# Kernel optimization log

Measured on AMD Instinct MI355X. Metric: run time of the kernel, lower is better.

The kernel has to match this reference:

```python
import jax, jax.numpy as jnp
import numpy as np

N = 64          # SSM state size
L = 8192        # l_max / sequence length
BATCH = 2048


def setup_inputs() -> dict:
    key = jax.random.key(0)
    k1, k2, k3, k4, k5 = jax.random.split(key, 5)
    u = jax.random.normal(k1, (BATCH, L), dtype=jnp.float32)
    # lecun_normal: std = 1/sqrt(fan_in), fan_in = dim -2
    A = jax.random.normal(k2, (N, N), dtype=jnp.float32) / np.sqrt(N)
    B = jax.random.normal(k3, (N, 1), dtype=jnp.float32) / np.sqrt(N)
    C = jax.random.normal(k4, (1, N), dtype=jnp.float32)  # fan_in = 1
    D = jnp.ones((1,), dtype=jnp.float32)
    # log_step_initializer: log-uniform over [1e-3, 1e-1]
    lo, hi = np.log(0.001), np.log(0.1)
    log_step = (jax.random.uniform(k5, (1,)) * (hi - lo) + lo).astype(jnp.float32)
    return {"u": u, "A": A, "B": B, "C": C, "D": D, "log_step": log_step}


def _ssm_forward(u, A, B, C, D, log_step):
    n_state = A.shape[0]
    seq_len = u.shape[-1]
    step = jnp.exp(log_step)  # (1,)
    # Bilinear discretization: Ab = (I - s/2 A)^-1 (I + s/2 A); Bb = s (I - s/2 A)^-1 B
    I = jnp.eye(n_state, dtype=A.dtype)
    half = (step / 2.0) * A
    BL = jnp.linalg.inv(I - half)
    Ab = BL @ (I + half)            # (N, N)
    Bb = (step * BL) @ B            # (N, 1)
    # K_conv: K[l] = C @ Ab^l @ Bb, computed with a scan (x_{l+1} = Ab x_l)
    def kstep(x, _):
        y = (C @ x)[0]              # scalar
        return Ab @ x, y
    _, K = jax.lax.scan(kstep, Bb[:, 0], None, length=seq_len)  # (L,)
    # Causal convolution via FFT with zero padding to 2L (matches jnp.pad + rfft)
    nfft = 2 * seq_len
    ud = jnp.fft.rfft(u, n=nfft, axis=-1)    # (BATCH, L+1) complex
    Kd = jnp.fft.rfft(K, n=nfft)             # (L+1,) complex, shared over batch
    y = jnp.fft.irfft(ud * Kd, n=nfft, axis=-1)[..., :seq_len]
    return y + D * u


def reference(u, A, B, C, D, log_step):
    return _ssm_forward(u, A, B, C, D, log_step)
```

## Files before the change

kernel.cpp:

```cpp
#include <hip/hip_runtime.h>
#include <math.h>

#define LSEQ   8192
#define CHUNK  64
#define NCHUNK 128
#define NBATCH 2048
#define NGRP   16
#define GLEN   8

#define WS_E   0
#define WS_SG  (NBATCH * NGRP * 64)
#define T0     (NBATCH * NCHUNK * 64)
#define WS_WH  (T0 + 8256)
#define WS_WL  (T0 + 12352)
#define WS_PH  (T0 + 16448)
#define WS_PL  (T0 + 18496)
#define WS_A1H (T0 + 20544)
#define WS_A1L (T0 + 22592)
#define WS_PGH (T0 + 24640)
#define WS_PGL (T0 + 26688)

typedef short bf16x8 __attribute__((ext_vector_type(8)));
typedef float f32x4  __attribute__((ext_vector_type(4)));
typedef unsigned short u16;

__device__ __forceinline__ u16 bf16rne(float x) {
  unsigned b = __builtin_bit_cast(unsigned, x);
  return (u16)((b + 0x7fffu + ((b >> 16) & 1u)) >> 16);
}
__device__ __forceinline__ float bf2f(u16 h) {
  return __builtin_bit_cast(float, ((unsigned)h) << 16);
}
__device__ __forceinline__ void split2(float x, u16& h, u16& l) {
  h = bf16rne(x);
  l = bf16rne(x - bf2f(h));
}
__device__ __forceinline__ void split3(float x, u16& h, u16& m, u16& l) {
  h = bf16rne(x);
  float r = x - bf2f(h);
  m = bf16rne(r);
  r -= bf2f(m);
  l = bf16rne(r);
}

__device__ __forceinline__ int sinv(int c) {
  return (c & 0x23) | ((c & 4) << 2) | ((c & 0x18) >> 1);
}

__device__ __forceinline__ int swz(int r, int c) {
  return r * 64 + (c ^ ((r & 7) << 3));
}
__device__ __forceinline__ float tri_get(const u16* p, int r, int c) {
  const int e = swz(r, c);
  return bf2f(p[e]) + bf2f(p[4096 + e]) + bf2f(p[8192 + e]);
}

__device__ __forceinline__ void mfma_tile3(
    const u16* __restrict__ A3, const u16* __restrict__ B3, u16* __restrict__ D3,
    int mt, int nt, int aShift,
    const u16* add1, const u16* add2, int addI, int rLo, int rHi) {
  const int lane = threadIdx.x & 63;
  const int n = lane & 15, q = lane >> 4;
  int ar = mt * 16 + n - aShift;
  ar = ar < 0 ? 0 : (ar > 63 ? 63 : ar);
  const int bc = nt * 16 + n;
  bf16x8 ah[2], am[2], al[2], bh[2], bm[2], bl[2];
#pragma unroll
  for (int ks = 0; ks < 2; ++ks) {
    const int ao = swz(ar, ks * 32 + q * 8);
    const int bo = swz(bc, ks * 32 + q * 8);
    ah[ks] = *(const bf16x8*)(A3 + ao);
    am[ks] = *(const bf16x8*)(A3 + 4096 + ao);
    al[ks] = *(const bf16x8*)(A3 + 8192 + ao);
    bh[ks] = *(const bf16x8*)(B3 + bo);
    bm[ks] = *(const bf16x8*)(B3 + 4096 + bo);
    bl[ks] = *(const bf16x8*)(B3 + 8192 + bo);
  }
  f32x4 acc = {0.f, 0.f, 0.f, 0.f};
#define MF(a, b) acc = __builtin_amdgcn_mfma_f32_16x16x32_bf16(a, b, acc, 0, 0, 0)
  MF(ah[0], bh[0]); MF(ah[1], bh[1]);
  MF(ah[0], bm[0]); MF(ah[1], bm[1]);
  MF(am[0], bh[0]); MF(am[1], bh[1]);
  MF(ah[0], bl[0]); MF(ah[1], bl[1]);
  MF(am[0], bm[0]); MF(am[1], bm[1]);
  MF(al[0], bh[0]); MF(al[1], bh[1]);
#undef MF
#pragma unroll
  for (int j = 0; j < 4; ++j) {
    const int i = mt * 16 + q * 4 + j, c = nt * 16 + n;
    float v = acc[j];
    if (add1) v += tri_get(add1, i, c);
    if (add2) v += tri_get(add2, i, c);
    if (addI && i == c) v += 1.f;
    if (i >= rLo && i < rHi) {
      u16 h3, m3, l3; split3(v, h3, m3, l3);
      const int e = swz(i, c);
      D3[e] = h3; D3[4096 + e] = m3; D3[8192 + e] = l3;
    }
  }
}

__device__ __forceinline__ void pair_phase(
    const u16* Pf, const u16* Qt, u16* Fn, u16* Tn,
    const u16* addF1, const u16* addT1, int addI) {
  __syncthreads();
  const int w = threadIdx.x >> 6;
#pragma unroll
  for (int tix = w; tix < 32; tix += 16) {
    if (tix < 16) mfma_tile3(Pf, Qt, Fn, tix >> 2, tix & 3, 0, addF1, 0, addI, 0, 64);
    else { const int s = tix - 16; mfma_tile3(Qt, Pf, Tn, s >> 2, s & 3, 0, addT1, 0, addI, 0, 64); }
  }
}
__device__ __forceinline__ void single_phase(
    const u16* A3, const u16* B3, u16* D3,
    const u16* add1, const u16* add2, int addI) {
  __syncthreads();
  const int w = threadIdx.x >> 6;
  mfma_tile3(A3, B3, D3, w >> 2, w & 3, 0, add1, add2, addI, 0, 64);
}

__global__ void __launch_bounds__(1024)
ssm_pre(const float* __restrict__ Ag, const float* __restrict__ Bg,
        const float* __restrict__ Cg, const float* __restrict__ Dg,
        const float* __restrict__ lsg, float* __restrict__ ws) {
  __shared__ __attribute__((aligned(16))) u16 TRI[6][3 * 4096];
  __shared__ float Kl[64];
  u16* tri0 = TRI[0]; u16* tri1 = TRI[1]; u16* tri2 = TRI[2];
  u16* tri3 = TRI[3]; u16* tri4 = TRI[4]; u16* tri5 = TRI[5];

  const int t = threadIdx.x;
  const int w = t >> 6;
  const float step = expf(lsg[0]);
  const float hstep = 0.5f * step;
  const float D0 = Dg[0];

  float* Xf = (float*)tri2;
  for (int e = t; e < 4096; e += 1024) {
    const float x = hstep * Ag[e];
    Xf[e] = x;
    u16 h3, m3, l3; split3(x, h3, m3, l3);
    const int s = swz(e >> 6, e & 63);
    tri0[s] = h3; tri0[4096 + s] = m3; tri0[8192 + s] = l3;
  }
  __syncthreads();
  for (int e = t; e < 4096; e += 1024) {
    const int r = e >> 6, c = e & 63;
    const float x = Xf[c * 64 + r];
    u16 h3, m3, l3; split3(x, h3, m3, l3);
    const int s = swz(r, c);
    tri1[s] = h3; tri1[4096 + s] = m3; tri1[8192 + s] = l3;
  }
  pair_phase(tri0, tri1, tri2, tri3, 0, 0, 0);
  pair_phase(tri2, tri3, tri4, tri5, 0, 0, 0);
  single_phase(tri4, tri3, tri0, tri4, tri2, 1);
  single_phase(tri3, tri4, tri2, tri3, tri5, 1);
  pair_phase(tri0, tri1, tri3, tri5, tri0, tri2, 0);
  pair_phase(tri3, tri1, tri4, tri2, tri3, tri5, 0);

  __syncthreads();
  if (t < 64) {
    float acc = 0.f;
    for (int m = 0; m < 64; ++m) acc += tri_get(tri3, t, m) * Bg[m];
    const float bb = step * acc;
    u16 h3, m3, l3; split3(bb, h3, m3, l3);
    const int s = swz(0, t);
    tri0[s] = h3; tri0[4096 + s] = m3; tri0[8192 + s] = l3;
  } else if (t < 128) {
    const int r = t - 64;
    float acc = 0.f;
    for (int m = 0; m < 64; ++m) acc += tri_get(tri2, r, m) * Cg[m];
    u16 h3, m3, l3; split3(acc, h3, m3, l3);
    const int s = swz(0, r);
    tri1[s] = h3; tri1[4096 + s] = m3; tri1[8192 + s] = l3;
  }

  u16 *curF = tri4, *curT = tri2, *nxtF = tri3, *nxtT = tri5;
  for (int k = 1; k <= 32; k <<= 1) {
    __syncthreads();
    const int mtLo = k >> 4, mtHi = (2 * k - 1) >> 4;
    const int cnt = (mtHi - mtLo + 1) * 4;
    const int total = 32 + 2 * cnt;
    for (int tix = w; tix < total; tix += 16) {
      if (tix < 16) {
        mfma_tile3(curF, curT, nxtF, tix >> 2, tix & 3, 0, 0, 0, 0, 0, 64);
      } else if (tix < 32) {
        const int s = tix - 16;
        mfma_tile3(curT, curF, nxtT, s >> 2, s & 3, 0, 0, 0, 0, 0, 64);
      } else if (tix < 32 + cnt) {
        const int s = tix - 32;
        mfma_tile3(tri0, curF, tri0, mtLo + (s >> 2), s & 3, k, 0, 0, 0, k, 2 * k);
      } else {
        const int s = tix - 32 - cnt;
        mfma_tile3(tri1, curT, tri1, mtLo + (s >> 2), s & 3, k, 0, 0, 0, k, 2 * k);
      }
    }
    u16* tmp;
    tmp = curF; curF = nxtF; nxtF = tmp;
    tmp = curT; curT = nxtT; nxtT = tmp;
  }

  __syncthreads();
  u16* ph  = (u16*)(ws + WS_PH);
  u16* pl  = (u16*)(ws + WS_PL);
  u16* a1h = (u16*)(ws + WS_A1H);
  u16* a1l = (u16*)(ws + WS_A1L);
  u16* pgh = (u16*)(ws + WS_PGH);
  u16* pgl = (u16*)(ws + WS_PGL);
  for (int e = t; e < 4096; e += 1024) {
    const int r = e >> 6, c = e & 63;
    const float x = tri_get(curF, r, sinv(c));
    u16 hh, ll; split2(x, hh, ll); ph[e] = hh; pl[e] = ll;
  }
  for (int r2 = 0; r2 < 3; ++r2) {
    pair_phase(curF, curT, nxtF, nxtT, 0, 0, 0);
    u16* tmp;
    tmp = curF; curF = nxtF; nxtF = tmp;
    tmp = curT; curT = nxtT; nxtT = tmp;
  }
  __syncthreads();
  for (int e = t; e < 4096; e += 1024) {
    const int r = e >> 6, c = e & 63, ci = sinv(c);
    float x = tri_get(curF, r, ci);
    u16 hh, ll; split2(x, hh, ll); pgh[e] = hh; pgl[e] = ll;
    const float a1v = tri_get(tri1, r, ci);
    split2(a1v, hh, ll); a1h[e] = hh; a1l[e] = ll;
  }
  if (t < 64) {
    float acc = 0.f;
    for (int m = 0; m < 64; ++m) acc += Cg[m] * tri_get(tri0, t, m);
    Kl[t] = acc;
  }
  __syncthreads();
  u16* wh = (u16*)(ws + WS_WH);
  u16* wl = (u16*)(ws + WS_WL);
  for (int e = t; e < 8192; e += 1024) {
    const int i = e >> 6, j = e & 63;
    float wv;
    if (i < 64) wv = ((i >= j) ? Kl[i - j] : 0.f) + ((i == j) ? D0 : 0.f);
    else        wv = tri_get(tri0, 63 - j, i - 64);
    u16 hh, ll; split2(wv, hh, ll);
    wh[e] = hh;
    wl[e] = ll;
  }
}


__device__ __forceinline__ void acc_to_bfrag(const f32x4* accS,
                                             bf16x8* Sbh, bf16x8* Sbl) {
#pragma unroll
  for (int mt = 0; mt < 4; ++mt)
#pragma unroll
    for (int j = 0; j < 4; ++j) {
      u16 hh, ll; split2(accS[mt][j], hh, ll);
      Sbh[mt >> 1][(mt & 1) * 4 + j] = (short)hh;
      Sbl[mt >> 1][(mt & 1) * 4 + j] = (short)ll;
    }
}

__global__ void __launch_bounds__(256, 2)
ssm_scan_e(float* __restrict__ ws, const float* __restrict__ u) {
  const int lane = threadIdx.x & 63;
  const int n = lane & 15, q = lane >> 4;
  const int wid = blockIdx.x * 4 + (threadIdx.x >> 6);
  const int R = (wid >> 4) * 16;
  const int g = wid & 15;

  const u16* ph = (const u16*)(ws + WS_PH);
  const u16* pl = (const u16*)(ws + WS_PL);
  const u16* wh = (const u16*)(ws + WS_WH);
  const u16* wl = (const u16*)(ws + WS_WL);
  bf16x8 Ph[4][2], Pl[4][2], Wbh[4][2], Wbl[4][2];
#pragma unroll
  for (int mt = 0; mt < 4; ++mt)
#pragma unroll
    for (int ks = 0; ks < 2; ++ks) {
      const int off  = (mt * 16 + n) * 64 + ks * 32 + q * 8;
      const int offb = off + 64 * 64;
      Ph[mt][ks]  = *(const bf16x8*)(ph + off);
      Pl[mt][ks]  = *(const bf16x8*)(pl + off);
      Wbh[mt][ks] = *(const bf16x8*)(wh + offb);
      Wbl[mt][ks] = *(const bf16x8*)(wl + offb);
    }

  bf16x8 Sbh[2], Sbl[2];
#pragma unroll
  for (int ks = 0; ks < 2; ++ks)
#pragma unroll
    for (int j = 0; j < 8; ++j) { Sbh[ks][j] = 0; Sbl[ks][j] = 0; }

  const int cb = g * GLEN;
  const float* ub = u + (size_t)(R + n) * LSEQ + cb * 64 + q * 8;

  f32x4 f0 = *(const f32x4*)(ub);
  f32x4 f1 = *(const f32x4*)(ub + 4);
  f32x4 f2 = *(const f32x4*)(ub + 32);
  f32x4 f3 = *(const f32x4*)(ub + 36);

  for (int c8 = 0; c8 < GLEN; ++c8) {
    bf16x8 ubh[2], ubl[2];
    {
      float xs0[8] = {f0[0], f0[1], f0[2], f0[3], f1[0], f1[1], f1[2], f1[3]};
      float xs1[8] = {f2[0], f2[1], f2[2], f2[3], f3[0], f3[1], f3[2], f3[3]};
#pragma unroll
      for (int j = 0; j < 8; ++j) {
        u16 hh, ll;
        split2(xs0[j], hh, ll); ubh[0][j] = (short)hh; ubl[0][j] = (short)ll;
        split2(xs1[j], hh, ll); ubh[1][j] = (short)hh; ubl[1][j] = (short)ll;
      }
    }
    const int cn = (c8 + 1 < GLEN) ? (c8 + 1) : c8;
    const float* nb = ub + cn * 64;
    f0 = *(const f32x4*)(nb);
    f1 = *(const f32x4*)(nb + 4);
    f2 = *(const f32x4*)(nb + 32);
    f3 = *(const f32x4*)(nb + 36);

    f32x4 accS[4];
#pragma unroll
    for (int mt = 0; mt < 4; ++mt) {
      f32x4 as = {0.f, 0.f, 0.f, 0.f};
#define MF(a, b) as = __builtin_amdgcn_mfma_f32_16x16x32_bf16(a, b, as, 0, 0, 0)
      MF(Wbh[mt][0], ubh[0]); MF(Wbh[mt][1], ubh[1]);
      MF(Wbh[mt][0], ubl[0]); MF(Wbh[mt][1], ubl[1]);
      MF(Wbl[mt][0], ubh[0]); MF(Wbl[mt][1], ubh[1]);
      MF(Ph[mt][0], Sbh[0]);  MF(Ph[mt][1], Sbh[1]);
      MF(Ph[mt][0], Sbl[0]);  MF(Ph[mt][1], Sbl[1]);
      MF(Pl[mt][0], Sbh[0]);  MF(Pl[mt][1], Sbh[1]);
#undef MF
      accS[mt] = as;
    }

    if (c8 + 1 < GLEN) {
      acc_to_bfrag(accS, Sbh, Sbl);
    } else {
      float* eb = ws + WS_E + ((size_t)(R + n) * NGRP + g) * 64 + q * 4;
#pragma unroll
      for (int mt = 0; mt < 4; ++mt)
        *(f32x4*)(eb + mt * 16) = accS[mt];
    }
    __builtin_amdgcn_sched_barrier(0);
  }
}

__global__ void __launch_bounds__(256, 2)
ssm_scan_sg(float* __restrict__ ws) {
  const int lane = threadIdx.x & 63;
  const int n = lane & 15, q = lane >> 4;
  const int wid = blockIdx.x * 4 + (threadIdx.x >> 6);
  const int R = wid * 16;

  const u16* pgh = (const u16*)(ws + WS_PGH);
  const u16* pgl = (const u16*)(ws + WS_PGL);
  bf16x8 Ph[4][2], Pl[4][2];
#pragma unroll
  for (int mt = 0; mt < 4; ++mt)
#pragma unroll
    for (int ks = 0; ks < 2; ++ks) {
      int off = (mt * 16 + n) * 64 + ks * 32 + q * 8;
      Ph[mt][ks] = *(const bf16x8*)(pgh + off);
      Pl[mt][ks] = *(const bf16x8*)(pgl + off);
    }

  bf16x8 Sbh[2], Sbl[2];
#pragma unroll
  for (int ks = 0; ks < 2; ++ks)
#pragma unroll
    for (int j = 0; j < 8; ++j) { Sbh[ks][j] = 0; Sbl[ks][j] = 0; }

  const float* erow = ws + WS_E + ((size_t)(R + n) * NGRP) * 64 + q * 4;
  float*       srow = ws + WS_SG + ((size_t)(R + n) * NGRP) * 64 + q * 4;

  {
    f32x4 z = {0.f, 0.f, 0.f, 0.f};
#pragma unroll
    for (int mt = 0; mt < 4; ++mt) *(f32x4*)(srow + mt * 16) = z;
  }

  f32x4 ec[4];
#pragma unroll
  for (int mt = 0; mt < 4; ++mt) ec[mt] = *(const f32x4*)(erow + mt * 16);

  for (int g = 0; g < NGRP - 1; ++g) {
    const int gn = (g + 1 < NGRP - 1) ? (g + 1) : g;
    f32x4 en[4];
#pragma unroll
    for (int mt = 0; mt < 4; ++mt)
      en[mt] = *(const f32x4*)(erow + (size_t)gn * 64 + mt * 16);

    f32x4 accS[4];
#pragma unroll
    for (int mt = 0; mt < 4; ++mt) {
      f32x4 as = ec[mt];
#define MF(a, b) as = __builtin_amdgcn_mfma_f32_16x16x32_bf16(a, b, as, 0, 0, 0)
      MF(Ph[mt][0], Sbh[0]); MF(Ph[mt][1], Sbh[1]);
      MF(Ph[mt][0], Sbl[0]); MF(Ph[mt][1], Sbl[1]);
      MF(Pl[mt][0], Sbh[0]); MF(Pl[mt][1], Sbh[1]);
#undef MF
      accS[mt] = as;
    }

#pragma unroll
    for (int mt = 0; mt < 4; ++mt)
      *(f32x4*)(srow + (size_t)(g + 1) * 64 + mt * 16) = accS[mt];

    if (g + 1 < NGRP - 1) acc_to_bfrag(accS, Sbh, Sbl);
    __builtin_amdgcn_sched_barrier(0);

    ec[0] = en[0]; ec[1] = en[1]; ec[2] = en[2]; ec[3] = en[3];
  }
}

__global__ void __launch_bounds__(256, 2)
ssm_scan_main(const float* __restrict__ ws, const float* __restrict__ u,
              float* __restrict__ y) {
  __shared__ __attribute__((aligned(16))) u16 WT[2][4096];
  __shared__ __attribute__((aligned(16))) u16 A1S[2][4096];
  const int lane = threadIdx.x & 63;
  const int n = lane & 15, q = lane >> 4;
  const int wid = blockIdx.x * 4 + (threadIdx.x >> 6);
  const int R = (wid >> 4) * 16;
  const int g = wid & 15;

  {
    const u16* whg  = (const u16*)(ws + WS_WH);
    const u16* wlg  = (const u16*)(ws + WS_WL);
    const u16* a1hg = (const u16*)(ws + WS_A1H);
    const u16* a1lg = (const u16*)(ws + WS_A1L);
    for (int e = threadIdx.x; e < 4096; e += 256) {
      const int s = swz(e >> 6, e & 63);
      WT[0][s]  = whg[e];  WT[1][s]  = wlg[e];
      A1S[0][s] = a1hg[e]; A1S[1][s] = a1lg[e];
    }
  }

  const u16* ph = (const u16*)(ws + WS_PH);
  const u16* pl = (const u16*)(ws + WS_PL);
  const u16* wh = (const u16*)(ws + WS_WH);
  const u16* wl = (const u16*)(ws + WS_WL);
  bf16x8 Ph[4][2], Pl[4][2], Wbh[4][2], Wbl[4][2];
#pragma unroll
  for (int mt = 0; mt < 4; ++mt)
#pragma unroll
    for (int ks = 0; ks < 2; ++ks) {
      const int off  = (mt * 16 + n) * 64 + ks * 32 + q * 8;
      const int offb = off + 64 * 64;
      Ph[mt][ks]  = *(const bf16x8*)(ph + off);
      Pl[mt][ks]  = *(const bf16x8*)(pl + off);
      Wbh[mt][ks] = *(const bf16x8*)(wh + offb);
      Wbl[mt][ks] = *(const bf16x8*)(wl + offb);
    }

  bf16x8 Sbh[2], Sbl[2];
  {
    const float* sgp = ws + WS_SG + ((size_t)(R + n) * NGRP + g) * 64;
#pragma unroll
    for (int ks = 0; ks < 2; ++ks) {
      f32x4 s0 = *(const f32x4*)(sgp + ks * 32 + q * 4);
      f32x4 s1 = *(const f32x4*)(sgp + ks * 32 + 16 + q * 4);
#pragma unroll
      for (int j = 0; j < 4; ++j) {
        u16 hh, ll;
        split2(s0[j], hh, ll); Sbh[ks][j] = (short)hh; Sbl[ks][j] = (short)ll;
        split2(s1[j], hh, ll); Sbh[ks][j + 4] = (short)hh; Sbl[ks][j + 4] = (short)ll;
      }
    }
  }

  const int cb = g * GLEN;
  const float* ub = u + (size_t)(R + n) * LSEQ + cb * 64 + q * 8;
  float*     yrow = y + (size_t)(R + n) * LSEQ + q * 4;

  f32x4 f0 = *(const f32x4*)(ub);
  f32x4 f1 = *(const f32x4*)(ub + 4);
  f32x4 f2 = *(const f32x4*)(ub + 32);
  f32x4 f3 = *(const f32x4*)(ub + 36);

  __syncthreads();

  for (int c8 = 0; c8 < GLEN; ++c8) {
    const int c = cb + c8;
    bf16x8 ubh[2], ubl[2];
    {
      float xs0[8] = {f0[0], f0[1], f0[2], f0[3], f1[0], f1[1], f1[2], f1[3]};
      float xs1[8] = {f2[0], f2[1], f2[2], f2[3], f3[0], f3[1], f3[2], f3[3]};
#pragma unroll
      for (int j = 0; j < 8; ++j) {
        u16 hh, ll;
        split2(xs0[j], hh, ll); ubh[0][j] = (short)hh; ubl[0][j] = (short)ll;
        split2(xs1[j], hh, ll); ubh[1][j] = (short)hh; ubl[1][j] = (short)ll;
      }
    }
    const int cn = (c8 + 1 < GLEN) ? (c8 + 1) : c8;
    const float* nb = ub + cn * 64;
    f0 = *(const f32x4*)(nb);
    f1 = *(const f32x4*)(nb + 4);
    f2 = *(const f32x4*)(nb + 32);
    f3 = *(const f32x4*)(nb + 36);

#pragma unroll
    for (int mt = 0; mt < 4; ++mt) {
      f32x4 ay = {0.f, 0.f, 0.f, 0.f};
      const int o0 = swz(mt * 16 + n, q * 8);
      const int o1 = swz(mt * 16 + n, 32 + q * 8);
      bf16x8 th0 = *(const bf16x8*)(&WT[0][o0]);
      bf16x8 th1 = *(const bf16x8*)(&WT[0][o1]);
      bf16x8 tl0 = *(const bf16x8*)(&WT[1][o0]);
      bf16x8 tl1 = *(const bf16x8*)(&WT[1][o1]);
#define MF(a, b) ay = __builtin_amdgcn_mfma_f32_16x16x32_bf16(a, b, ay, 0, 0, 0)
      MF(th0, ubh[0]); MF(th1, ubh[1]);
      MF(th0, ubl[0]); MF(th1, ubl[1]);
      MF(tl0, ubh[0]); MF(tl1, ubh[1]);
      bf16x8 ah0 = *(const bf16x8*)(&A1S[0][o0]);
      bf16x8 ah1 = *(const bf16x8*)(&A1S[0][o1]);
      bf16x8 al0 = *(const bf16x8*)(&A1S[1][o0]);
      bf16x8 al1 = *(const bf16x8*)(&A1S[1][o1]);
      MF(ah0, Sbh[0]); MF(ah1, Sbh[1]);
      MF(ah0, Sbl[0]); MF(ah1, Sbl[1]);
      MF(al0, Sbh[0]); MF(al1, Sbh[1]);
#undef MF
      *(f32x4*)(yrow + (size_t)c * 64 + mt * 16) = ay;
    }

    if (c8 + 1 < GLEN) {
      f32x4 accS[4];
#pragma unroll
      for (int mt = 0; mt < 4; ++mt) {
        f32x4 as = {0.f, 0.f, 0.f, 0.f};
#define MF(a, b) as = __builtin_amdgcn_mfma_f32_16x16x32_bf16(a, b, as, 0, 0, 0)
        MF(Wbh[mt][0], ubh[0]); MF(Wbh[mt][1], ubh[1]);
        MF(Wbh[mt][0], ubl[0]); MF(Wbh[mt][1], ubl[1]);
        MF(Wbl[mt][0], ubh[0]); MF(Wbl[mt][1], ubh[1]);
        MF(Ph[mt][0], Sbh[0]);  MF(Ph[mt][1], Sbh[1]);
        MF(Ph[mt][0], Sbl[0]);  MF(Ph[mt][1], Sbl[1]);
        MF(Pl[mt][0], Sbh[0]);  MF(Pl[mt][1], Sbh[1]);
#undef MF
        accS[mt] = as;
      }
      acc_to_bfrag(accS, Sbh, Sbl);
    }
    __builtin_amdgcn_sched_barrier(0);
  }
}

extern "C" void kernel_launch(void* const* d_in, const int* in_sizes, int n_in,
                              void* d_out, int out_size, void* d_ws, size_t ws_size,
                              hipStream_t stream) {
  const float* u  = (const float*)d_in[0];
  const float* A  = (const float*)d_in[1];
  const float* B  = (const float*)d_in[2];
  const float* C  = (const float*)d_in[3];
  const float* D  = (const float*)d_in[4];
  const float* ls = (const float*)d_in[5];
  float* ws  = (float*)d_ws;
  float* out = (float*)d_out;

  ssm_pre<<<dim3(1), dim3(1024), 0, stream>>>(A, B, C, D, ls, ws);
  ssm_scan_e<<<dim3(512), dim3(256), 0, stream>>>(ws, u);
  ssm_scan_sg<<<dim3(32), dim3(256), 0, stream>>>(ws);
  ssm_scan_main<<<dim3(512), dim3(256), 0, stream>>>(ws, u, out);
}
```

Baseline: 207.3 us.

## Fold inter-group state scan into main kernel, drop separate scan kernel

Removes the serial 32-block inter-group carry kernel and instead has each main-kernel wave recompute its own starting state by scanning the group end-states of all preceding groups with MFMA. The last group also skips computing its unused end state in the chunk-end kernel. This eliminates one launch and a low-parallelism serial stage, but adds redundant work: wave g repeats g scan steps, up to 15, before its main loop.

```diff
diff --git a/kernel.cpp b/kernel.cpp
--- a/kernel.cpp
+++ b/kernel.cpp
@@ -9,7 +9,6 @@
 #define GLEN   8
 
 #define WS_E   0
-#define WS_SG  (NBATCH * NGRP * 64)
 #define T0     (NBATCH * NCHUNK * 64)
 #define WS_WH  (T0 + 8256)
 #define WS_WL  (T0 + 12352)
@@ -264,6 +263,7 @@
   const int wid = blockIdx.x * 4 + (threadIdx.x >> 6);
   const int R = (wid >> 4) * 16;
   const int g = wid & 15;
+  if (g == NGRP - 1) return;
 
   const u16* ph = (const u16*)(ws + WS_PH);
   const u16* pl = (const u16*)(ws + WS_PL);
@@ -343,74 +343,6 @@
 }
 
 __global__ void __launch_bounds__(256, 2)
-ssm_scan_sg(float* __restrict__ ws) {
-  const int lane = threadIdx.x & 63;
-  const int n = lane & 15, q = lane >> 4;
-  const int wid = blockIdx.x * 4 + (threadIdx.x >> 6);
-  const int R = wid * 16;
-
-  const u16* pgh = (const u16*)(ws + WS_PGH);
-  const u16* pgl = (const u16*)(ws + WS_PGL);
-  bf16x8 Ph[4][2], Pl[4][2];
-#pragma unroll
-  for (int mt = 0; mt < 4; ++mt)
-#pragma unroll
-    for (int ks = 0; ks < 2; ++ks) {
-      int off = (mt * 16 + n) * 64 + ks * 32 + q * 8;
-      Ph[mt][ks] = *(const bf16x8*)(pgh + off);
-      Pl[mt][ks] = *(const bf16x8*)(pgl + off);
-    }
-
-  bf16x8 Sbh[2], Sbl[2];
-#pragma unroll
-  for (int ks = 0; ks < 2; ++ks)
-#pragma unroll
-    for (int j = 0; j < 8; ++j) { Sbh[ks][j] = 0; Sbl[ks][j] = 0; }
-
-  const float* erow = ws + WS_E + ((size_t)(R + n) * NGRP) * 64 + q * 4;
-  float*       srow = ws + WS_SG + ((size_t)(R + n) * NGRP) * 64 + q * 4;
-
-  {
-    f32x4 z = {0.f, 0.f, 0.f, 0.f};
-#pragma unroll
-    for (int mt = 0; mt < 4; ++mt) *(f32x4*)(srow + mt * 16) = z;
-  }
-
-  f32x4 ec[4];
-#pragma unroll
-  for (int mt = 0; mt < 4; ++mt) ec[mt] = *(const f32x4*)(erow + mt * 16);
-
-  for (int g = 0; g < NGRP - 1; ++g) {
-    const int gn = (g + 1 < NGRP - 1) ? (g + 1) : g;
-    f32x4 en[4];
-#pragma unroll
-    for (int mt = 0; mt < 4; ++mt)
-      en[mt] = *(const f32x4*)(erow + (size_t)gn * 64 + mt * 16);
-
-    f32x4 accS[4];
-#pragma unroll
-    for (int mt = 0; mt < 4; ++mt) {
-      f32x4 as = ec[mt];
-#define MF(a, b) as = __builtin_amdgcn_mfma_f32_16x16x32_bf16(a, b, as, 0, 0, 0)
-      MF(Ph[mt][0], Sbh[0]); MF(Ph[mt][1], Sbh[1]);
-      MF(Ph[mt][0], Sbl[0]); MF(Ph[mt][1], Sbl[1]);
-      MF(Pl[mt][0], Sbh[0]); MF(Pl[mt][1], Sbh[1]);
-#undef MF
-      accS[mt] = as;
-    }
-
-#pragma unroll
-    for (int mt = 0; mt < 4; ++mt)
-      *(f32x4*)(srow + (size_t)(g + 1) * 64 + mt * 16) = accS[mt];
-
-    if (g + 1 < NGRP - 1) acc_to_bfrag(accS, Sbh, Sbl);
-    __builtin_amdgcn_sched_barrier(0);
-
-    ec[0] = en[0]; ec[1] = en[1]; ec[2] = en[2]; ec[3] = en[3];
-  }
-}
-
-__global__ void __launch_bounds__(256, 2)
 ssm_scan_main(const float* __restrict__ ws, const float* __restrict__ u,
               float* __restrict__ y) {
   __shared__ __attribute__((aligned(16))) u16 WT[2][4096];
@@ -433,6 +365,39 @@
     }
   }
 
+  f32x4 sAcc[4];
+#pragma unroll
+  for (int mt = 0; mt < 4; ++mt) sAcc[mt] = f32x4{0.f, 0.f, 0.f, 0.f};
+  if (g > 0) {
+    const u16* pgh = (const u16*)(ws + WS_PGH);
+    const u16* pgl = (const u16*)(ws + WS_PGL);
+    bf16x8 PGh[4][2], PGl[4][2];
+#pragma unroll
+    for (int mt = 0; mt < 4; ++mt)
+#pragma unroll
+      for (int ks = 0; ks < 2; ++ks) {
+        const int off = (mt * 16 + n) * 64 + ks * 32 + q * 8;
+        PGh[mt][ks] = *(const bf16x8*)(pgh + off);
+        PGl[mt][ks] = *(const bf16x8*)(pgl + off);
+      }
+    const float* erow = ws + WS_E + ((size_t)(R + n) * NGRP) * 64 + q * 4;
+    bf16x8 Sh[2], Sl[2];
+    for (int j = 0; j < g; ++j) {
+      acc_to_bfrag(sAcc, Sh, Sl);
+#pragma unroll
+      for (int mt = 0; mt < 4; ++mt) {
+        f32x4 as = *(const f32x4*)(erow + (size_t)j * 64 + mt * 16);
+#define MF(a, b) as = __builtin_amdgcn_mfma_f32_16x16x32_bf16(a, b, as, 0, 0, 0)
+        MF(PGh[mt][0], Sh[0]); MF(PGh[mt][1], Sh[1]);
+        MF(PGh[mt][0], Sl[0]); MF(PGh[mt][1], Sl[1]);
+        MF(PGl[mt][0], Sh[0]); MF(PGl[mt][1], Sh[1]);
+#undef MF
+        sAcc[mt] = as;
+      }
+      __builtin_amdgcn_sched_barrier(0);
+    }
+  }
+
   const u16* ph = (const u16*)(ws + WS_PH);
   const u16* pl = (const u16*)(ws + WS_PL);
   const u16* wh = (const u16*)(ws + WS_WH);
@@ -451,20 +416,7 @@
     }
 
   bf16x8 Sbh[2], Sbl[2];
-  {
-    const float* sgp = ws + WS_SG + ((size_t)(R + n) * NGRP + g) * 64;
-#pragma unroll
-    for (int ks = 0; ks < 2; ++ks) {
-      f32x4 s0 = *(const f32x4*)(sgp + ks * 32 + q * 4);
-      f32x4 s1 = *(const f32x4*)(sgp + ks * 32 + 16 + q * 4);
-#pragma unroll
-      for (int j = 0; j < 4; ++j) {
-        u16 hh, ll;
-        split2(s0[j], hh, ll); Sbh[ks][j] = (short)hh; Sbl[ks][j] = (short)ll;
-        split2(s1[j], hh, ll); Sbh[ks][j + 4] = (short)hh; Sbl[ks][j + 4] = (short)ll;
-      }
-    }
-  }
+  acc_to_bfrag(sAcc, Sbh, Sbl);
 
   const int cb = g * GLEN;
   const float* ub = u + (size_t)(R + n) * LSEQ + cb * 64 + q * 8;
@@ -556,6 +508,5 @@
 
   ssm_pre<<<dim3(1), dim3(1024), 0, stream>>>(A, B, C, D, ls, ws);
   ssm_scan_e<<<dim3(512), dim3(256), 0, stream>>>(ws, u);
-  ssm_scan_sg<<<dim3(32), dim3(256), 0, stream>>>(ws);
   ssm_scan_main<<<dim3(512), dim3(256), 0, stream>>>(ws, u, out);
 }
```

Measured after the change: 214.4 us. 1.03x slower.

## Software-pipeline input projection off the serial state chain and skip unused last group

Applied to the files above, without the earlier changes.

Each loop iteration previously ran the input-projection MFMAs (W*u) and the state-propagation MFMAs (P*S) as one chain. Now the input projection for the next chunk is computed ahead and used as the starting accumulator, so only the state MFMAs stay on the serial dependency. The sched_barrier is removed, the loop is marked unroll 1, and in the end-state pass the last group's warps exit early because their end state is presumably never read. This shortens the loop-carried critical path and gives the compiler more room to overlap independent MFMAs, at the cost of holding extra registers for vC.

```diff
diff --git a/kernel.cpp b/kernel.cpp
--- a/kernel.cpp
+++ b/kernel.cpp
@@ -257,6 +257,34 @@
     }
 }
 
+__device__ __forceinline__ void split_u(const f32x4& f0, const f32x4& f1,
+                                        const f32x4& f2, const f32x4& f3,
+                                        bf16x8* ubh, bf16x8* ubl) {
+  float xs0[8] = {f0[0], f0[1], f0[2], f0[3], f1[0], f1[1], f1[2], f1[3]};
+  float xs1[8] = {f2[0], f2[1], f2[2], f2[3], f3[0], f3[1], f3[2], f3[3]};
+#pragma unroll
+  for (int j = 0; j < 8; ++j) {
+    u16 hh, ll;
+    split2(xs0[j], hh, ll); ubh[0][j] = (short)hh; ubl[0][j] = (short)ll;
+    split2(xs1[j], hh, ll); ubh[1][j] = (short)hh; ubl[1][j] = (short)ll;
+  }
+}
+
+__device__ __forceinline__ void calc_v(const bf16x8 Wbh[4][2], const bf16x8 Wbl[4][2],
+                                       const bf16x8* ubh, const bf16x8* ubl,
+                                       f32x4* vC) {
+#pragma unroll
+  for (int mt = 0; mt < 4; ++mt) {
+    f32x4 as = {0.f, 0.f, 0.f, 0.f};
+#define MF(a, b) as = __builtin_amdgcn_mfma_f32_16x16x32_bf16(a, b, as, 0, 0, 0)
+    MF(Wbh[mt][0], ubh[0]); MF(Wbh[mt][1], ubh[1]);
+    MF(Wbh[mt][0], ubl[0]); MF(Wbh[mt][1], ubl[1]);
+    MF(Wbl[mt][0], ubh[0]); MF(Wbl[mt][1], ubh[1]);
+#undef MF
+    vC[mt] = as;
+  }
+}
+
 __global__ void __launch_bounds__(256, 2)
 ssm_scan_e(float* __restrict__ ws, const float* __restrict__ u) {
   const int lane = threadIdx.x & 63;
@@ -264,6 +292,7 @@
   const int wid = blockIdx.x * 4 + (threadIdx.x >> 6);
   const int R = (wid >> 4) * 16;
   const int g = wid & 15;
+  if (g == NGRP - 1) return;
 
   const u16* ph = (const u16*)(ws + WS_PH);
   const u16* pl = (const u16*)(ws + WS_PL);
@@ -295,42 +324,36 @@
   f32x4 f1 = *(const f32x4*)(ub + 4);
   f32x4 f2 = *(const f32x4*)(ub + 32);
   f32x4 f3 = *(const f32x4*)(ub + 36);
-
+  bf16x8 ubh[2], ubl[2];
+  split_u(f0, f1, f2, f3, ubh, ubl);
+  f32x4 vC[4];
+  calc_v(Wbh, Wbl, ubh, ubl, vC);
+
+#pragma unroll 1
   for (int c8 = 0; c8 < GLEN; ++c8) {
-    bf16x8 ubh[2], ubl[2];
-    {
-      float xs0[8] = {f0[0], f0[1], f0[2], f0[3], f1[0], f1[1], f1[2], f1[3]};
-      float xs1[8] = {f2[0], f2[1], f2[2], f2[3], f3[0], f3[1], f3[2], f3[3]};
-#pragma unroll
-      for (int j = 0; j < 8; ++j) {
-        u16 hh, ll;
-        split2(xs0[j], hh, ll); ubh[0][j] = (short)hh; ubl[0][j] = (short)ll;
-        split2(xs1[j], hh, ll); ubh[1][j] = (short)hh; ubl[1][j] = (short)ll;
-      }
-    }
-    const int cn = (c8 + 1 < GLEN) ? (c8 + 1) : c8;
-    const float* nb = ub + cn * 64;
-    f0 = *(const f32x4*)(nb);
-    f1 = *(const f32x4*)(nb + 4);
-    f2 = *(const f32x4*)(nb + 32);
-    f3 = *(const f32x4*)(nb + 36);
+    if (c8 + 1 < GLEN) {
+      const float* nb = ub + (c8 + 1) * 64;
+      f0 = *(const f32x4*)(nb);
+      f1 = *(const f32x4*)(nb + 4);
+      f2 = *(const f32x4*)(nb + 32);
+      f3 = *(const f32x4*)(nb + 36);
+    }
 
     f32x4 accS[4];
 #pragma unroll
     for (int mt = 0; mt < 4; ++mt) {
-      f32x4 as = {0.f, 0.f, 0.f, 0.f};
+      f32x4 as = vC[mt];
 #define MF(a, b) as = __builtin_amdgcn_mfma_f32_16x16x32_bf16(a, b, as, 0, 0, 0)
-      MF(Wbh[mt][0], ubh[0]); MF(Wbh[mt][1], ubh[1]);
-      MF(Wbh[mt][0], ubl[0]); MF(Wbh[mt][1], ubl[1]);
-      MF(Wbl[mt][0], ubh[0]); MF(Wbl[mt][1], ubh[1]);
-      MF(Ph[mt][0], Sbh[0]);  MF(Ph[mt][1], Sbh[1]);
-      MF(Ph[mt][0], Sbl[0]);  MF(Ph[mt][1], Sbl[1]);
-      MF(Pl[mt][0], Sbh[0]);  MF(Pl[mt][1], Sbh[1]);
+      MF(Ph[mt][0], Sbh[0]); MF(Ph[mt][1], Sbh[1]);
+      MF(Ph[mt][0], Sbl[0]); MF(Ph[mt][1], Sbl[1]);
+      MF(Pl[mt][0], Sbh[0]); MF(Pl[mt][1], Sbh[1]);
 #undef MF
       accS[mt] = as;
     }
 
     if (c8 + 1 < GLEN) {
+      split_u(f0, f1, f2, f3, ubh, ubl);
+      calc_v(Wbh, Wbl, ubh, ubl, vC);
       acc_to_bfrag(accS, Sbh, Sbl);
     } else {
       float* eb = ws + WS_E + ((size_t)(R + n) * NGRP + g) * 64 + q * 4;
@@ -338,7 +361,6 @@
       for (int mt = 0; mt < 4; ++mt)
         *(f32x4*)(eb + mt * 16) = accS[mt];
     }
-    __builtin_amdgcn_sched_barrier(0);
   }
 }
 
@@ -474,28 +496,23 @@
   f32x4 f1 = *(const f32x4*)(ub + 4);
   f32x4 f2 = *(const f32x4*)(ub + 32);
   f32x4 f3 = *(const f32x4*)(ub + 36);
-
-  __syncthreads();
-
+  bf16x8 ubh[2], ubl[2];
+  split_u(f0, f1, f2, f3, ubh, ubl);
+  f32x4 vC[4];
+  calc_v(Wbh, Wbl, ubh, ubl, vC);
+
+  __syncthreads();
+
+#pragma unroll 1
   for (int c8 = 0; c8 < GLEN; ++c8) {
     const int c = cb + c8;
-    bf16x8 ubh[2], ubl[2];
-    {
-      float xs0[8] = {f0[0], f0[1], f0[2], f0[3], f1[0], f1[1], f1[2], f1[3]};
-      float xs1[8] = {f2[0], f2[1], f2[2], f2[3], f3[0], f3[1], f3[2], f3[3]};
-#pragma unroll
-      for (int j = 0; j < 8; ++j) {
-        u16 hh, ll;
-        split2(xs0[j], hh, ll); ubh[0][j] = (short)hh; ubl[0][j] = (short)ll;
-        split2(xs1[j], hh, ll); ubh[1][j] = (short)hh; ubl[1][j] = (short)ll;
-      }
-    }
-    const int cn = (c8 + 1 < GLEN) ? (c8 + 1) : c8;
-    const float* nb = ub + cn * 64;
-    f0 = *(const f32x4*)(nb);
-    f1 = *(const f32x4*)(nb + 4);
-    f2 = *(const f32x4*)(nb + 32);
-    f3 = *(const f32x4*)(nb + 36);
+    if (c8 + 1 < GLEN) {
+      const float* nb = ub + (c8 + 1) * 64;
+      f0 = *(const f32x4*)(nb);
+      f1 = *(const f32x4*)(nb + 4);
+      f2 = *(const f32x4*)(nb + 32);
+      f3 = *(const f32x4*)(nb + 36);
+    }
 
 #pragma unroll
     for (int mt = 0; mt < 4; ++mt) {
@@ -525,20 +542,18 @@
       f32x4 accS[4];
 #pragma unroll
       for (int mt = 0; mt < 4; ++mt) {
-        f32x4 as = {0.f, 0.f, 0.f, 0.f};
+        f32x4 as = vC[mt];
 #define MF(a, b) as = __builtin_amdgcn_mfma_f32_16x16x32_bf16(a, b, as, 0, 0, 0)
-        MF(Wbh[mt][0], ubh[0]); MF(Wbh[mt][1], ubh[1]);
-        MF(Wbh[mt][0], ubl[0]); MF(Wbh[mt][1], ubl[1]);
-        MF(Wbl[mt][0], ubh[0]); MF(Wbl[mt][1], ubh[1]);
-        MF(Ph[mt][0], Sbh[0]);  MF(Ph[mt][1], Sbh[1]);
-        MF(Ph[mt][0], Sbl[0]);  MF(Ph[mt][1], Sbl[1]);
-        MF(Pl[mt][0], Sbh[0]);  MF(Pl[mt][1], Sbh[1]);
+        MF(Ph[mt][0], Sbh[0]); MF(Ph[mt][1], Sbh[1]);
+        MF(Ph[mt][0], Sbl[0]); MF(Ph[mt][1], Sbl[1]);
+        MF(Pl[mt][0], Sbh[0]); MF(Pl[mt][1], Sbh[1]);
 #undef MF
         accS[mt] = as;
       }
+      split_u(f0, f1, f2, f3, ubh, ubl);
+      calc_v(Wbh, Wbl, ubh, ubl, vC);
       acc_to_bfrag(accS, Sbh, Sbl);
     }
-    __builtin_amdgcn_sched_barrier(0);
   }
 }
 
```

Result: slower. 271.8 us (+31.1%).
